# Kernel optimization log

Measured on AMD Instinct MI355X. Metric: run time of the kernel, lower is better.

The kernel has to match this reference:

```python
import jax, jax.numpy as jnp
import numpy as np

NEG_SLOPE = 0.2


def gat_conv(x, src, dst, W, att_src, att_dst, bias, heads, out_dim, concat):
    N = x.shape[0]
    h = (x @ W).reshape(N, heads, out_dim)              # [N,H,F]
    a_src = (h * att_src[None]).sum(-1)                 # [N,H]
    a_dst = (h * att_dst[None]).sum(-1)                 # [N,H]
    e = jax.nn.leaky_relu(a_src[src] + a_dst[dst], NEG_SLOPE)  # [E,H]
    # segment softmax over incoming edges of each dst node
    m = jax.ops.segment_max(e, dst, num_segments=N)     # [N,H]
    p = jnp.exp(e - m[dst])
    s = jax.ops.segment_sum(p, dst, num_segments=N)     # [N,H]
    alpha = p / (s[dst] + 1e-16)                        # [E,H]
    msg = h[src] * alpha[:, :, None]                    # [E,H,F]
    agg = jax.ops.segment_sum(msg, dst, num_segments=N) # [N,H,F]
    if concat:
        out = agg.reshape(N, heads * out_dim)
    else:
        out = agg.mean(axis=1)
    return out + bias


def gat_forward(x, edge_index, W1, att_src1, att_dst1, b1, W2, att_src2, att_dst2, b2):
    N = x.shape[0]
    # add self loops (PyG GATConv default)
    loops = jnp.arange(N, dtype=edge_index.dtype)
    src = jnp.concatenate([edge_index[0], loops])
    dst = jnp.concatenate([edge_index[1], loops])
    h = gat_conv(x, src, dst, W1, att_src1, att_dst1, b1, heads=8, out_dim=8, concat=True)
    h = jax.nn.elu(h)
    # dropout is identity in eval mode
    num_class = W2.shape[1]
    o = gat_conv(h, src, dst, W2, att_src2, att_dst2, b2, heads=1, out_dim=num_class, concat=True)
    return jax.nn.log_softmax(o, axis=-1)


def setup_inputs() -> dict:
    key = jax.random.key(0)
    ks = jax.random.split(key, 8)
    N, E, F_in, C = 100000, 1600000, 128, 40
    H, F_h = 8, 8
    x = jax.random.normal(ks[0], (N, F_in), dtype=jnp.float32)
    edge_index = jax.random.randint(ks[1], (2, E), 0, N, dtype=jnp.int64)
    sc = lambda f: 1.0 / np.sqrt(f)
    W1 = jax.random.normal(ks[2], (F_in, H * F_h), dtype=jnp.float32) * sc(F_in)
    att_src1 = jax.random.normal(ks[3], (H, F_h), dtype=jnp.float32) * sc(F_h)
    att_dst1 = jax.random.normal(ks[4], (H, F_h), dtype=jnp.float32) * sc(F_h)
    b1 = jnp.zeros((H * F_h,), dtype=jnp.float32)
    W2 = jax.random.normal(ks[5], (H * F_h, C), dtype=jnp.float32) * sc(H * F_h)
    att_src2 = jax.random.normal(ks[6], (1, C), dtype=jnp.float32) * sc(C)
    att_dst2 = jax.random.normal(ks[7], (1, C), dtype=jnp.float32) * sc(C)
    b2 = jnp.zeros((C,), dtype=jnp.float32)
    return {"x": x, "edge_index": edge_index, "W1": W1, "att_src1": att_src1,
            "att_dst1": att_dst1, "b1": b1, "W2": W2, "att_src2": att_src2,
            "att_dst2": att_dst2, "b2": b2}


def reference(x, edge_index, W1, att_src1, att_dst1, b1, W2, att_src2, att_dst2, b2):
    return gat_forward(x, edge_index, W1, att_src1, att_dst1, b1, W2, att_src2, att_dst2, b2)
```

## Files before the change

kernel.cpp:

```cpp
#include <hip/hip_runtime.h>
#include <math.h>

#define NEG_SLOPE 0.2f

typedef __attribute__((ext_vector_type(8))) short short8;
typedef __attribute__((ext_vector_type(4))) float f32x4;

__device__ __forceinline__ float leaky(float x) { return x > 0.f ? x : NEG_SLOPE * x; }

__device__ __forceinline__ short f2bf(float f) {
    union { float f; unsigned u; } v; v.f = f;
    unsigned r = v.u + 0x7fffu + ((v.u >> 16) & 1u);
    return (short)(r >> 16);
}
__device__ __forceinline__ float bf2f(unsigned short s) {
    union { unsigned u; float f; } v; v.u = ((unsigned)s) << 16;
    return v.f;
}
__device__ __forceinline__ void unpack2(unsigned v, float& lo, float& hi) {
    union { unsigned u; float f; } a, b;
    a.u = v << 16; b.u = v & 0xffff0000u;
    lo = a.f; hi = b.f;
}

#define GCHUNK 256
#define NB_MAX 1024

__global__ __launch_bounds__(256) void hist_kernel(const int* __restrict__ dst, int E, int nbuck,
                                                   int* __restrict__ histG, int* __restrict__ total) {
    __shared__ int lh[NB_MAX];
    int g = blockIdx.x, t = threadIdx.x;
    for (int i = t; i < nbuck; i += 256) lh[i] = 0;
    __syncthreads();
    int ce = (E + GCHUNK - 1) / GCHUNK;
    int e0 = g * ce, e1 = min(e0 + ce, E);
    for (int e = e0 + t; e < e1; e += 256)
        atomicAdd(&lh[dst[e] >> 7], 1);
    __syncthreads();
    for (int i = t; i < nbuck; i += 256) {
        histG[i * GCHUNK + g] = lh[i];
        if (lh[i]) atomicAdd(&total[i], lh[i]);
    }
}

__global__ __launch_bounds__(1024) void bscan_kernel(const int* __restrict__ total,
                                                     int* __restrict__ bbase, int nbuck) {
    __shared__ int sh[1024];
    int t = threadIdx.x;
    int v = (t < nbuck) ? total[t] : 0;
    sh[t] = v; __syncthreads();
    for (int s = 1; s < 1024; s <<= 1) {
        int add = (t >= s) ? sh[t - s] : 0;
        __syncthreads();
        sh[t] += add;
        __syncthreads();
    }
    if (t < nbuck) bbase[t] = sh[t] - v;
    if (t == nbuck - 1) bbase[nbuck] = sh[t];
}

__global__ __launch_bounds__(256) void bstart_kernel(const int* __restrict__ histG,
                                                     const int* __restrict__ bbase,
                                                     int* __restrict__ startG, int nbuck) {
    __shared__ int sh[256];
    int b = blockIdx.x, t = threadIdx.x;
    int v = histG[b * GCHUNK + t];
    sh[t] = v; __syncthreads();
    for (int s = 1; s < 256; s <<= 1) {
        int add = (t >= s) ? sh[t - s] : 0;
        __syncthreads();
        sh[t] += add;
        __syncthreads();
    }
    startG[b * GCHUNK + t] = bbase[b] + sh[t] - v;
}

__global__ __launch_bounds__(256) void bucket_scatter(const int* __restrict__ src,
                                                      const int* __restrict__ dst, int E, int nbuck,
                                                      const int* __restrict__ startG,
                                                      int* __restrict__ pairbuf) {
    __shared__ int cur[NB_MAX];
    int g = blockIdx.x, t = threadIdx.x;
    for (int i = t; i < nbuck; i += 256) cur[i] = startG[i * GCHUNK + g];
    __syncthreads();
    int ce = (E + GCHUNK - 1) / GCHUNK;
    int e0 = g * ce, e1 = min(e0 + ce, E);
    for (int e = e0 + t; e < e1; e += 256) {
        int d = dst[e], b = d >> 7;
        int pos = atomicAdd(&cur[b], 1);
        pairbuf[pos] = (src[e] << 7) | (d & 127);
    }
}

__global__ __launch_bounds__(256) void bucket_place(const int* __restrict__ pairbuf,
                                                    const int* __restrict__ bbase, int nbuck, int N,
                                                    int* __restrict__ deg, int* __restrict__ off,
                                                    int* __restrict__ csr) {
    __shared__ int stash[4096];
    __shared__ int ldeg[128], lcur[128], sh[128];
    int b = blockIdx.x, t = threadIdx.x;
    int p0 = bbase[b], p1 = bbase[b + 1];
    int cnt = p1 - p0;
    int node0 = b << 7;
    for (int i = t; i < 128; i += 256) ldeg[i] = 0;
    __syncthreads();
    for (int i = t; i < cnt; i += 256) {
        int pr = pairbuf[p0 + i];
        if (i < 4096) stash[i] = pr;
        atomicAdd(&ldeg[pr & 127], 1);
    }
    __syncthreads();
    if (t < 128) sh[t] = ldeg[t];
    __syncthreads();
    for (int s = 1; s < 128; s <<= 1) {
        int add = (t >= s && t < 128) ? sh[t - s] : 0;
        __syncthreads();
        if (t < 128) sh[t] += add;
        __syncthreads();
    }
    if (t < 128) {
        int excl = sh[t] - ldeg[t];
        int n = node0 + t;
        if (n < N) { deg[n] = ldeg[t]; off[n] = p0 + excl; }
        lcur[t] = p0 + excl;
    }
    __syncthreads();
    for (int i = t; i < cnt; i += 256) {
        int pr = (i < 4096) ? stash[i] : pairbuf[p0 + i];
        int pos = atomicAdd(&lcur[pr & 127], 1);
        csr[pos] = ((unsigned)pr) >> 7;
    }
}

__global__ __launch_bounds__(256) void gemm1_mfma(
    const float* __restrict__ x, const float* __restrict__ W1,
    const float* __restrict__ att_src, const float* __restrict__ att_dst,
    unsigned short* __restrict__ h1, float* __restrict__ a_src, float* __restrict__ a_dst, int N)
{
    __shared__ short Bl[16 * 64 * 8];
    __shared__ float Cs[4][32 * 64];
    int tid = threadIdx.x;
    for (int f0 = tid; f0 < 1024; f0 += 256) {
        int lane = f0 & 63, s = (f0 >> 6) & 3, ct = f0 >> 8;
        int kb = s * 32 + ((lane >> 4) << 3);
        int col = ct * 16 + (lane & 15);
        short* dp = &Bl[f0 * 8];
#pragma unroll
        for (int j = 0; j < 8; ++j) dp[j] = f2bf(W1[(kb + j) * 64 + col]);
    }
    __syncthreads();

    int lane = tid & 63, w = tid >> 6;
    int row0 = blockIdx.x * 128 + w * 32;
    int ra = min(row0 + (lane & 15), N - 1);
    int rb = min(row0 + 16 + (lane & 15), N - 1);
    const float* pa = x + (size_t)ra * 128 + ((lane >> 4) << 3);
    const float* pb = x + (size_t)rb * 128 + ((lane >> 4) << 3);

    f32x4 acc[2][4];
#pragma unroll
    for (int i = 0; i < 2; ++i)
#pragma unroll
        for (int j = 0; j < 4; ++j) acc[i][j] = (f32x4){0.f, 0.f, 0.f, 0.f};

#pragma unroll
    for (int s = 0; s < 4; ++s) {
        float4 a0 = *(const float4*)(pa + s * 32);
        float4 a1 = *(const float4*)(pa + s * 32 + 4);
        float4 c0 = *(const float4*)(pb + s * 32);
        float4 c1 = *(const float4*)(pb + s * 32 + 4);
        short8 af, cf;
        af[0] = f2bf(a0.x); af[1] = f2bf(a0.y); af[2] = f2bf(a0.z); af[3] = f2bf(a0.w);
        af[4] = f2bf(a1.x); af[5] = f2bf(a1.y); af[6] = f2bf(a1.z); af[7] = f2bf(a1.w);
        cf[0] = f2bf(c0.x); cf[1] = f2bf(c0.y); cf[2] = f2bf(c0.z); cf[3] = f2bf(c0.w);
        cf[4] = f2bf(c1.x); cf[5] = f2bf(c1.y); cf[6] = f2bf(c1.z); cf[7] = f2bf(c1.w);
#pragma unroll
        for (int ct = 0; ct < 4; ++ct) {
            short8 wf = *(const short8*)&Bl[((ct * 4 + s) * 64 + lane) * 8];
            acc[0][ct] = __builtin_amdgcn_mfma_f32_16x16x32_bf16(af, wf, acc[0][ct], 0, 0, 0);
            acc[1][ct] = __builtin_amdgcn_mfma_f32_16x16x32_bf16(cf, wf, acc[1][ct], 0, 0, 0);
        }
    }

    float* cs = &Cs[w][0];
#pragma unroll
    for (int rt = 0; rt < 2; ++rt)
#pragma unroll
        for (int ct = 0; ct < 4; ++ct)
#pragma unroll
            for (int r = 0; r < 4; ++r) {
                int row = rt * 16 + ((lane >> 4) << 2) + r;
                int col = ct * 16 + (lane & 15);
                cs[row * 64 + col] = acc[rt][ct][r];
            }
    __syncthreads();

    float asv = att_src[lane], adv = att_dst[lane];
    for (int r = 0; r < 32; ++r) {
        int row = row0 + r;
        float v = cs[r * 64 + lane];
        float ts = v * asv, td = v * adv;
        ts += __shfl_xor(ts, 1); ts += __shfl_xor(ts, 2); ts += __shfl_xor(ts, 4);
        td += __shfl_xor(td, 1); td += __shfl_xor(td, 2); td += __shfl_xor(td, 4);
        if (row < N) {
            h1[(size_t)row * 64 + lane] = (unsigned short)f2bf(v);
            if ((lane & 7) == 0) {
                a_src[row * 8 + (lane >> 3)] = ts;
                a_dst[row * 8 + (lane >> 3)] = td;
            }
        }
    }
}

__global__ __launch_bounds__(256) void agg1_kernel(
    const unsigned short* __restrict__ h1, const float* __restrict__ a_src, const float* __restrict__ a_dst,
    const int* __restrict__ off, const int* __restrict__ deg, const int* __restrict__ csr,
    const float* __restrict__ b1, unsigned short* __restrict__ helu, int N)
{
    int tid = threadIdx.x;
    int n = (blockIdx.x * 256 + tid) >> 6;
    int lane = tid & 63;
    if (n >= N) return;
    int o = off[n], d = deg[n];
    int h8 = lane & 7, g = lane >> 3;

    float adst = a_dst[n * 8 + h8];
    float pself = __expf(leaky(a_src[n * 8 + h8] + adst));
    float s = (g == 0) ? pself : 0.f;

    float aself = (g == 0) ? __shfl(pself, h8) : 0.f;
    uint4 dvs = *(const uint4*)(h1 + (size_t)n * 64 + h8 * 8);
    float lo, hi;
    float acc0, acc1, acc2, acc3, acc4, acc5, acc6, acc7;
    unpack2(dvs.x, lo, hi); acc0 = aself * lo; acc1 = aself * hi;
    unpack2(dvs.y, lo, hi); acc2 = aself * lo; acc3 = aself * hi;
    unpack2(dvs.z, lo, hi); acc4 = aself * lo; acc5 = aself * hi;
    unpack2(dvs.w, lo, hi); acc6 = aself * lo; acc7 = aself * hi;

    for (int base = 0; base < d; base += 64) {
        int idx = base + lane;
        int sv = (idx < d) ? csr[o + idx] : 0;
        int lim = min(64, d - base);
        int tmax2 = (((lim + 7) >> 3) + 1) & ~1;
        for (int t = 0; t < tmax2; t += 2) {
            int e0 = t * 8 + g, e1 = e0 + 8;
            int s0 = __shfl(sv, e0), s1 = __shfl(sv, e1);
            float as0 = a_src[s0 * 8 + h8];
            float as1 = a_src[s1 * 8 + h8];
            uint4 d0 = *(const uint4*)(h1 + (size_t)s0 * 64 + h8 * 8);
            uint4 d1 = *(const uint4*)(h1 + (size_t)s1 * 64 + h8 * 8);
            float p0 = (e0 < lim) ? __expf(leaky(as0 + adst)) : 0.f;
            float p1 = (e1 < lim) ? __expf(leaky(as1 + adst)) : 0.f;
            s += p0 + p1;
            unpack2(d0.x, lo, hi); acc0 = fmaf(p0, lo, acc0); acc1 = fmaf(p0, hi, acc1);
            unpack2(d0.y, lo, hi); acc2 = fmaf(p0, lo, acc2); acc3 = fmaf(p0, hi, acc3);
            unpack2(d0.z, lo, hi); acc4 = fmaf(p0, lo, acc4); acc5 = fmaf(p0, hi, acc5);
            unpack2(d0.w, lo, hi); acc6 = fmaf(p0, lo, acc6); acc7 = fmaf(p0, hi, acc7);
            unpack2(d1.x, lo, hi); acc0 = fmaf(p1, lo, acc0); acc1 = fmaf(p1, hi, acc1);
            unpack2(d1.y, lo, hi); acc2 = fmaf(p1, lo, acc2); acc3 = fmaf(p1, hi, acc3);
            unpack2(d1.z, lo, hi); acc4 = fmaf(p1, lo, acc4); acc5 = fmaf(p1, hi, acc5);
            unpack2(d1.w, lo, hi); acc6 = fmaf(p1, lo, acc6); acc7 = fmaf(p1, hi, acc7);
        }
    }
    s += __shfl_xor(s, 8); s += __shfl_xor(s, 16); s += __shfl_xor(s, 32);
    acc0 += __shfl_xor(acc0, 8); acc0 += __shfl_xor(acc0, 16); acc0 += __shfl_xor(acc0, 32);
    acc1 += __shfl_xor(acc1, 8); acc1 += __shfl_xor(acc1, 16); acc1 += __shfl_xor(acc1, 32);
    acc2 += __shfl_xor(acc2, 8); acc2 += __shfl_xor(acc2, 16); acc2 += __shfl_xor(acc2, 32);
    acc3 += __shfl_xor(acc3, 8); acc3 += __shfl_xor(acc3, 16); acc3 += __shfl_xor(acc3, 32);
    acc4 += __shfl_xor(acc4, 8); acc4 += __shfl_xor(acc4, 16); acc4 += __shfl_xor(acc4, 32);
    acc5 += __shfl_xor(acc5, 8); acc5 += __shfl_xor(acc5, 16); acc5 += __shfl_xor(acc5, 32);
    acc6 += __shfl_xor(acc6, 8); acc6 += __shfl_xor(acc6, 16); acc6 += __shfl_xor(acc6, 32);
    acc7 += __shfl_xor(acc7, 8); acc7 += __shfl_xor(acc7, 16); acc7 += __shfl_xor(acc7, 32);

    if (g == 0) {
        float r = 1.f / s;
        float4 bA = *(const float4*)(b1 + h8 * 8);
        float4 bB = *(const float4*)(b1 + h8 * 8 + 4);
        float v0 = acc0 * r + bA.x, v1 = acc1 * r + bA.y;
        float v2 = acc2 * r + bA.z, v3 = acc3 * r + bA.w;
        float v4 = acc4 * r + bB.x, v5 = acc5 * r + bB.y;
        float v6 = acc6 * r + bB.z, v7 = acc7 * r + bB.w;
        v0 = (v0 > 0.f) ? v0 : (__expf(v0) - 1.f);
        v1 = (v1 > 0.f) ? v1 : (__expf(v1) - 1.f);
        v2 = (v2 > 0.f) ? v2 : (__expf(v2) - 1.f);
        v3 = (v3 > 0.f) ? v3 : (__expf(v3) - 1.f);
        v4 = (v4 > 0.f) ? v4 : (__expf(v4) - 1.f);
        v5 = (v5 > 0.f) ? v5 : (__expf(v5) - 1.f);
        v6 = (v6 > 0.f) ? v6 : (__expf(v6) - 1.f);
        v7 = (v7 > 0.f) ? v7 : (__expf(v7) - 1.f);
        uint4 st;
        st.x = ((unsigned)(unsigned short)f2bf(v0)) | (((unsigned)(unsigned short)f2bf(v1)) << 16);
        st.y = ((unsigned)(unsigned short)f2bf(v2)) | (((unsigned)(unsigned short)f2bf(v3)) << 16);
        st.z = ((unsigned)(unsigned short)f2bf(v4)) | (((unsigned)(unsigned short)f2bf(v5)) << 16);
        st.w = ((unsigned)(unsigned short)f2bf(v6)) | (((unsigned)(unsigned short)f2bf(v7)) << 16);
        *(uint4*)(helu + (size_t)n * 64 + h8 * 8) = st;
    }
}

__global__ __launch_bounds__(256) void gemm2_mfma(
    const unsigned short* __restrict__ hin, const float* __restrict__ W2,
    const float* __restrict__ att_src2, const float* __restrict__ att_dst2,
    unsigned short* __restrict__ h2p, float* __restrict__ a_src, float* __restrict__ a_dst, int N)
{
    __shared__ short Bl[6 * 64 * 8];
    __shared__ float Cs[4][32 * 48];
    int tid = threadIdx.x;
    for (int f0 = tid; f0 < 384; f0 += 256) {
        int lane = f0 & 63; int fr = f0 >> 6; int s = fr & 1, ct = fr >> 1;
        int kb = s * 32 + ((lane >> 4) << 3);
        int col = ct * 16 + (lane & 15);
        short* dp = &Bl[f0 * 8];
#pragma unroll
        for (int j = 0; j < 8; ++j) dp[j] = (col < 40) ? f2bf(W2[(kb + j) * 40 + col]) : (short)0;
    }
    __syncthreads();

    int lane = tid & 63, w = tid >> 6;
    int row0 = blockIdx.x * 128 + w * 32;
    int ra = min(row0 + (lane & 15), N - 1);
    int rb = min(row0 + 16 + (lane & 15), N - 1);
    const unsigned short* pa = hin + (size_t)ra * 64 + ((lane >> 4) << 3);
    const unsigned short* pb = hin + (size_t)rb * 64 + ((lane >> 4) << 3);

    f32x4 acc[2][3];
#pragma unroll
    for (int i = 0; i < 2; ++i)
#pragma unroll
        for (int j = 0; j < 3; ++j) acc[i][j] = (f32x4){0.f, 0.f, 0.f, 0.f};

#pragma unroll
    for (int s = 0; s < 2; ++s) {
        short8 af = *(const short8*)(pa + s * 32);
        short8 cf = *(const short8*)(pb + s * 32);
#pragma unroll
        for (int ct = 0; ct < 3; ++ct) {
            short8 wf = *(const short8*)&Bl[((ct * 2 + s) * 64 + lane) * 8];
            acc[0][ct] = __builtin_amdgcn_mfma_f32_16x16x32_bf16(af, wf, acc[0][ct], 0, 0, 0);
            acc[1][ct] = __builtin_amdgcn_mfma_f32_16x16x32_bf16(cf, wf, acc[1][ct], 0, 0, 0);
        }
    }

    float* cs = &Cs[w][0];
#pragma unroll
    for (int rt = 0; rt < 2; ++rt)
#pragma unroll
        for (int ct = 0; ct < 3; ++ct)
#pragma unroll
            for (int r = 0; r < 4; ++r) {
                int row = rt * 16 + ((lane >> 4) << 2) + r;
                int col = ct * 16 + (lane & 15);
                cs[row * 48 + col] = acc[rt][ct][r];
            }
    __syncthreads();

    float asv = (lane < 40) ? att_src2[lane] : 0.f;
    float adv = (lane < 40) ? att_dst2[lane] : 0.f;
    for (int r = 0; r < 32; ++r) {
        int row = row0 + r;
        float v = (lane < 48) ? cs[r * 48 + lane] : 0.f;
        float ts = (lane < 40) ? v * asv : 0.f;
        float td = (lane < 40) ? v * adv : 0.f;
        for (int st = 1; st < 64; st <<= 1) { ts += __shfl_xor(ts, st); td += __shfl_xor(td, st); }
        if (row < N) {
            h2p[(size_t)row * 64 + lane] = (unsigned short)f2bf(v);
            if (lane == 0) { a_src[row] = ts; a_dst[row] = td; }
        }
    }
}

__global__ __launch_bounds__(256) void agg2_kernel(
    const unsigned short* __restrict__ h2p, const float* __restrict__ a_src, const float* __restrict__ a_dst,
    const int* __restrict__ off, const int* __restrict__ deg, const int* __restrict__ csr,
    const float* __restrict__ b2, float* __restrict__ out, int N)
{
    int tid = threadIdx.x;
    int n = (blockIdx.x * 256 + tid) >> 6;
    int lane = tid & 63;
    if (n >= N) return;
    int o = off[n], d = deg[n];
    int h8 = lane & 7, g = lane >> 3;

    float adst = a_dst[n];
    float pself = __expf(leaky(a_src[n] + adst));
    float sp = (g == 0) ? pself : 0.f;

    float aself = (g == 0) ? pself : 0.f;
    uint4 dvs = *(const uint4*)(h2p + (size_t)n * 64 + h8 * 8);
    float lo, hi;
    float acc0, acc1, acc2, acc3, acc4, acc5, acc6, acc7;
    unpack2(dvs.x, lo, hi); acc0 = aself * lo; acc1 = aself * hi;
    unpack2(dvs.y, lo, hi); acc2 = aself * lo; acc3 = aself * hi;
    unpack2(dvs.z, lo, hi); acc4 = aself * lo; acc5 = aself * hi;
    unpack2(dvs.w, lo, hi); acc6 = aself * lo; acc7 = aself * hi;

    for (int base = 0; base < d; base += 64) {
        int idx = base + lane;
        int sv = (idx < d) ? csr[o + idx] : 0;
        int lim = min(64, d - base);
        int tmax2 = (((lim + 7) >> 3) + 1) & ~1;
        for (int t = 0; t < tmax2; t += 2) {
            int e0 = t * 8 + g, e1 = e0 + 8;
            int s0 = __shfl(sv, e0), s1 = __shfl(sv, e1);
            float as0 = a_src[s0];
            float as1 = a_src[s1];
            uint4 d0 = *(const uint4*)(h2p + (size_t)s0 * 64 + h8 * 8);
            uint4 d1 = *(const uint4*)(h2p + (size_t)s1 * 64 + h8 * 8);
            float p0 = (e0 < lim) ? __expf(leaky(as0 + adst)) : 0.f;
            float p1 = (e1 < lim) ? __expf(leaky(as1 + adst)) : 0.f;
            sp += p0 + p1;
            unpack2(d0.x, lo, hi); acc0 = fmaf(p0, lo, acc0); acc1 = fmaf(p0, hi, acc1);
            unpack2(d0.y, lo, hi); acc2 = fmaf(p0, lo, acc2); acc3 = fmaf(p0, hi, acc3);
            unpack2(d0.z, lo, hi); acc4 = fmaf(p0, lo, acc4); acc5 = fmaf(p0, hi, acc5);
            unpack2(d0.w, lo, hi); acc6 = fmaf(p0, lo, acc6); acc7 = fmaf(p0, hi, acc7);
            unpack2(d1.x, lo, hi); acc0 = fmaf(p1, lo, acc0); acc1 = fmaf(p1, hi, acc1);
            unpack2(d1.y, lo, hi); acc2 = fmaf(p1, lo, acc2); acc3 = fmaf(p1, hi, acc3);
            unpack2(d1.z, lo, hi); acc4 = fmaf(p1, lo, acc4); acc5 = fmaf(p1, hi, acc5);
            unpack2(d1.w, lo, hi); acc6 = fmaf(p1, lo, acc6); acc7 = fmaf(p1, hi, acc7);
        }
    }
    sp += __shfl_xor(sp, 8); sp += __shfl_xor(sp, 16); sp += __shfl_xor(sp, 32);
    acc0 += __shfl_xor(acc0, 8); acc0 += __shfl_xor(acc0, 16); acc0 += __shfl_xor(acc0, 32);
    acc1 += __shfl_xor(acc1, 8); acc1 += __shfl_xor(acc1, 16); acc1 += __shfl_xor(acc1, 32);
    acc2 += __shfl_xor(acc2, 8); acc2 += __shfl_xor(acc2, 16); acc2 += __shfl_xor(acc2, 32);
    acc3 += __shfl_xor(acc3, 8); acc3 += __shfl_xor(acc3, 16); acc3 += __shfl_xor(acc3, 32);
    acc4 += __shfl_xor(acc4, 8); acc4 += __shfl_xor(acc4, 16); acc4 += __shfl_xor(acc4, 32);
    acc5 += __shfl_xor(acc5, 8); acc5 += __shfl_xor(acc5, 16); acc5 += __shfl_xor(acc5, 32);
    acc6 += __shfl_xor(acc6, 8); acc6 += __shfl_xor(acc6, 16); acc6 += __shfl_xor(acc6, 32);
    acc7 += __shfl_xor(acc7, 8); acc7 += __shfl_xor(acc7, 16); acc7 += __shfl_xor(acc7, 32);

    if (g == 0) {
        float r = 1.f / sp;
        float v0 = -INFINITY, v1 = -INFINITY, v2 = -INFINITY, v3 = -INFINITY;
        float v4 = -INFINITY, v5 = -INFINITY, v6 = -INFINITY, v7 = -INFINITY;
        if (h8 < 5) {
            float4 bA = *(const float4*)(b2 + h8 * 8);
            float4 bB = *(const float4*)(b2 + h8 * 8 + 4);
            v0 = acc0 * r + bA.x; v1 = acc1 * r + bA.y;
            v2 = acc2 * r + bA.z; v3 = acc3 * r + bA.w;
            v4 = acc4 * r + bB.x; v5 = acc5 * r + bB.y;
            v6 = acc6 * r + bB.z; v7 = acc7 * r + bB.w;
        }
        float mx = fmaxf(fmaxf(fmaxf(v0, v1), fmaxf(v2, v3)), fmaxf(fmaxf(v4, v5), fmaxf(v6, v7)));
        mx = fmaxf(mx, __shfl_xor(mx, 1));
        mx = fmaxf(mx, __shfl_xor(mx, 2));
        mx = fmaxf(mx, __shfl_xor(mx, 4));
        float se = 0.f;
        if (h8 < 5)
            se = __expf(v0 - mx) + __expf(v1 - mx) + __expf(v2 - mx) + __expf(v3 - mx)
               + __expf(v4 - mx) + __expf(v5 - mx) + __expf(v6 - mx) + __expf(v7 - mx);
        se += __shfl_xor(se, 1); se += __shfl_xor(se, 2); se += __shfl_xor(se, 4);
        if (h8 < 5) {
            float ls = mx + logf(se);
            float* op = out + (size_t)n * 40 + h8 * 8;
            *(float4*)op = make_float4(v0 - ls, v1 - ls, v2 - ls, v3 - ls);
            *(float4*)(op + 4) = make_float4(v4 - ls, v5 - ls, v6 - ls, v7 - ls);
        }
    }
}

extern "C" void kernel_launch(void* const* d_in, const int* in_sizes, int n_in,
                              void* d_out, int out_size, void* d_ws, size_t ws_size,
                              hipStream_t stream) {
    const float* x        = (const float*)d_in[0];
    const int*   ei       = (const int*)d_in[1];
    const float* W1       = (const float*)d_in[2];
    const float* att_src1 = (const float*)d_in[3];
    const float* att_dst1 = (const float*)d_in[4];
    const float* b1       = (const float*)d_in[5];
    const float* W2       = (const float*)d_in[6];
    const float* att_src2 = (const float*)d_in[7];
    const float* att_dst2 = (const float*)d_in[8];
    const float* b2       = (const float*)d_in[9];
    float* out = (float*)d_out;

    int N = in_sizes[0] / 128;
    int E = in_sizes[1] / 2;
    const int* src = ei;
    const int* dst = ei + E;
    int nbuck = (N + 127) >> 7;

    char* w = (char*)d_ws;
    auto alloc = [&](size_t bytes) { void* p = (void*)w; w += (bytes + 255) & ~(size_t)255; return p; };
    unsigned short* h1   = (unsigned short*)alloc((size_t)N * 64 * 2);
    unsigned short* helu = (unsigned short*)alloc((size_t)N * 64 * 2);
    float* as1  = (float*)alloc((size_t)N * 8 * 4);
    float* ad1  = (float*)alloc((size_t)N * 8 * 4);
    int*   degv = (int*)alloc((size_t)N * 4);
    int*   offv = (int*)alloc((size_t)(N + 1) * 4);
    int*   csr  = (int*)alloc((size_t)E * 4);
    int*   histG  = (int*)alloc((size_t)nbuck * GCHUNK * 4);
    int*   startG = (int*)alloc((size_t)nbuck * GCHUNK * 4);
    int*   total  = (int*)alloc((size_t)nbuck * 4);
    int*   bbase  = (int*)alloc((size_t)(nbuck + 1) * 4);
    int*   pairbuf = (int*)alloc((size_t)E * 4);
    unsigned short* h2p = h1;
    float* as2 = as1;
    float* ad2 = ad1;

    hipMemsetAsync(total, 0, (size_t)nbuck * 4, stream);
    hist_kernel<<<GCHUNK, 256, 0, stream>>>(dst, E, nbuck, histG, total);
    bscan_kernel<<<1, 1024, 0, stream>>>(total, bbase, nbuck);
    bstart_kernel<<<nbuck, 256, 0, stream>>>(histG, bbase, startG, nbuck);
    bucket_scatter<<<GCHUNK, 256, 0, stream>>>(src, dst, E, nbuck, startG, pairbuf);
    bucket_place<<<nbuck, 256, 0, stream>>>(pairbuf, bbase, nbuck, N, degv, offv, csr);

    int gb = (N + 127) / 128;
    gemm1_mfma<<<gb, 256, 0, stream>>>(x, W1, att_src1, att_dst1, h1, as1, ad1, N);
    agg1_kernel<<<(N + 3) / 4, 256, 0, stream>>>(h1, as1, ad1, offv, degv, csr, b1, helu, N);
    gemm2_mfma<<<gb, 256, 0, stream>>>(helu, W2, att_src2, att_dst2, h2p, as2, ad2, N);
    agg2_kernel<<<(N + 3) / 4, 256, 0, stream>>>(h2p, as2, ad2, offv, degv, csr, b2, out, N);
}
```

Measured before the change: 327.5 us.

## Map one graph node per half-wavefront in both aggregation kernels

Both aggregation kernels now give each destination node 32 lanes instead of a full 64-lane wavefront. There are 4 edge groups of 8 head or feature lanes, and the grid launches half as many blocks. With about 16 incoming edges per node, the old mapping left many lanes idle and spent a third butterfly-reduction stage. Packing two nodes per wavefront should raise lane utilization and cut shuffle work. The cost is a longer serial edge loop per group, plus an odd-step tail and a conditional self-loop load.

```diff
diff --git a/kernel.cpp b/kernel.cpp
--- a/kernel.cpp
+++ b/kernel.cpp
@@ -218,33 +218,38 @@
     const float* __restrict__ b1, unsigned short* __restrict__ helu, int N)
 {
     int tid = threadIdx.x;
-    int n = (blockIdx.x * 256 + tid) >> 6;
+    int n = (blockIdx.x * 256 + tid) >> 5;
     int lane = tid & 63;
+    int l32 = lane & 31;
+    int hb = lane & 32;
     if (n >= N) return;
     int o = off[n], d = deg[n];
-    int h8 = lane & 7, g = lane >> 3;
+    int h8 = l32 & 7, g = l32 >> 3;
 
     float adst = a_dst[n * 8 + h8];
     float pself = __expf(leaky(a_src[n * 8 + h8] + adst));
     float s = (g == 0) ? pself : 0.f;
 
-    float aself = (g == 0) ? __shfl(pself, h8) : 0.f;
-    uint4 dvs = *(const uint4*)(h1 + (size_t)n * 64 + h8 * 8);
     float lo, hi;
-    float acc0, acc1, acc2, acc3, acc4, acc5, acc6, acc7;
-    unpack2(dvs.x, lo, hi); acc0 = aself * lo; acc1 = aself * hi;
-    unpack2(dvs.y, lo, hi); acc2 = aself * lo; acc3 = aself * hi;
-    unpack2(dvs.z, lo, hi); acc4 = aself * lo; acc5 = aself * hi;
-    unpack2(dvs.w, lo, hi); acc6 = aself * lo; acc7 = aself * hi;
-
-    for (int base = 0; base < d; base += 64) {
-        int idx = base + lane;
+    float acc0 = 0.f, acc1 = 0.f, acc2 = 0.f, acc3 = 0.f;
+    float acc4 = 0.f, acc5 = 0.f, acc6 = 0.f, acc7 = 0.f;
+    if (g == 0) {
+        uint4 dvs = *(const uint4*)(h1 + (size_t)n * 64 + h8 * 8);
+        unpack2(dvs.x, lo, hi); acc0 = pself * lo; acc1 = pself * hi;
+        unpack2(dvs.y, lo, hi); acc2 = pself * lo; acc3 = pself * hi;
+        unpack2(dvs.z, lo, hi); acc4 = pself * lo; acc5 = pself * hi;
+        unpack2(dvs.w, lo, hi); acc6 = pself * lo; acc7 = pself * hi;
+    }
+
+    for (int base = 0; base < d; base += 32) {
+        int idx = base + l32;
         int sv = (idx < d) ? csr[o + idx] : 0;
-        int lim = min(64, d - base);
-        int tmax2 = (((lim + 7) >> 3) + 1) & ~1;
-        for (int t = 0; t < tmax2; t += 2) {
-            int e0 = t * 8 + g, e1 = e0 + 8;
-            int s0 = __shfl(sv, e0), s1 = __shfl(sv, e1);
+        int lim = min(32, d - base);
+        int tm = (lim + 3) >> 2;
+        int t = 0;
+        for (; t + 1 < tm; t += 2) {
+            int e0 = t * 4 + g, e1 = e0 + 4;
+            int s0 = __shfl(sv, hb | e0), s1 = __shfl(sv, hb | e1);
             float as0 = a_src[s0 * 8 + h8];
             float as1 = a_src[s1 * 8 + h8];
             uint4 d0 = *(const uint4*)(h1 + (size_t)s0 * 64 + h8 * 8);
@@ -261,16 +266,28 @@
             unpack2(d1.z, lo, hi); acc4 = fmaf(p1, lo, acc4); acc5 = fmaf(p1, hi, acc5);
             unpack2(d1.w, lo, hi); acc6 = fmaf(p1, lo, acc6); acc7 = fmaf(p1, hi, acc7);
         }
-    }
-    s += __shfl_xor(s, 8); s += __shfl_xor(s, 16); s += __shfl_xor(s, 32);
-    acc0 += __shfl_xor(acc0, 8); acc0 += __shfl_xor(acc0, 16); acc0 += __shfl_xor(acc0, 32);
-    acc1 += __shfl_xor(acc1, 8); acc1 += __shfl_xor(acc1, 16); acc1 += __shfl_xor(acc1, 32);
-    acc2 += __shfl_xor(acc2, 8); acc2 += __shfl_xor(acc2, 16); acc2 += __shfl_xor(acc2, 32);
-    acc3 += __shfl_xor(acc3, 8); acc3 += __shfl_xor(acc3, 16); acc3 += __shfl_xor(acc3, 32);
-    acc4 += __shfl_xor(acc4, 8); acc4 += __shfl_xor(acc4, 16); acc4 += __shfl_xor(acc4, 32);
-    acc5 += __shfl_xor(acc5, 8); acc5 += __shfl_xor(acc5, 16); acc5 += __shfl_xor(acc5, 32);
-    acc6 += __shfl_xor(acc6, 8); acc6 += __shfl_xor(acc6, 16); acc6 += __shfl_xor(acc6, 32);
-    acc7 += __shfl_xor(acc7, 8); acc7 += __shfl_xor(acc7, 16); acc7 += __shfl_xor(acc7, 32);
+        if (t < tm) {
+            int e0 = t * 4 + g;
+            int s0 = __shfl(sv, hb | e0);
+            float as0 = a_src[s0 * 8 + h8];
+            uint4 d0 = *(const uint4*)(h1 + (size_t)s0 * 64 + h8 * 8);
+            float p0 = (e0 < lim) ? __expf(leaky(as0 + adst)) : 0.f;
+            s += p0;
+            unpack2(d0.x, lo, hi); acc0 = fmaf(p0, lo, acc0); acc1 = fmaf(p0, hi, acc1);
+            unpack2(d0.y, lo, hi); acc2 = fmaf(p0, lo, acc2); acc3 = fmaf(p0, hi, acc3);
+            unpack2(d0.z, lo, hi); acc4 = fmaf(p0, lo, acc4); acc5 = fmaf(p0, hi, acc5);
+            unpack2(d0.w, lo, hi); acc6 = fmaf(p0, lo, acc6); acc7 = fmaf(p0, hi, acc7);
+        }
+    }
+    s += __shfl_xor(s, 8); s += __shfl_xor(s, 16);
+    acc0 += __shfl_xor(acc0, 8); acc0 += __shfl_xor(acc0, 16);
+    acc1 += __shfl_xor(acc1, 8); acc1 += __shfl_xor(acc1, 16);
+    acc2 += __shfl_xor(acc2, 8); acc2 += __shfl_xor(acc2, 16);
+    acc3 += __shfl_xor(acc3, 8); acc3 += __shfl_xor(acc3, 16);
+    acc4 += __shfl_xor(acc4, 8); acc4 += __shfl_xor(acc4, 16);
+    acc5 += __shfl_xor(acc5, 8); acc5 += __shfl_xor(acc5, 16);
+    acc6 += __shfl_xor(acc6, 8); acc6 += __shfl_xor(acc6, 16);
+    acc7 += __shfl_xor(acc7, 8); acc7 += __shfl_xor(acc7, 16);
 
     if (g == 0) {
         float r = 1.f / s;
@@ -374,33 +391,38 @@
     const float* __restrict__ b2, float* __restrict__ out, int N)
 {
     int tid = threadIdx.x;
-    int n = (blockIdx.x * 256 + tid) >> 6;
+    int n = (blockIdx.x * 256 + tid) >> 5;
     int lane = tid & 63;
+    int l32 = lane & 31;
+    int hb = lane & 32;
     if (n >= N) return;
     int o = off[n], d = deg[n];
-    int h8 = lane & 7, g = lane >> 3;
+    int h8 = l32 & 7, g = l32 >> 3;
 
     float adst = a_dst[n];
     float pself = __expf(leaky(a_src[n] + adst));
     float sp = (g == 0) ? pself : 0.f;
 
-    float aself = (g == 0) ? pself : 0.f;
-    uint4 dvs = *(const uint4*)(h2p + (size_t)n * 64 + h8 * 8);
     float lo, hi;
-    float acc0, acc1, acc2, acc3, acc4, acc5, acc6, acc7;
-    unpack2(dvs.x, lo, hi); acc0 = aself * lo; acc1 = aself * hi;
-    unpack2(dvs.y, lo, hi); acc2 = aself * lo; acc3 = aself * hi;
-    unpack2(dvs.z, lo, hi); acc4 = aself * lo; acc5 = aself * hi;
-    unpack2(dvs.w, lo, hi); acc6 = aself * lo; acc7 = aself * hi;
-
-    for (int base = 0; base < d; base += 64) {
-        int idx = base + lane;
+    float acc0 = 0.f, acc1 = 0.f, acc2 = 0.f, acc3 = 0.f;
+    float acc4 = 0.f, acc5 = 0.f, acc6 = 0.f, acc7 = 0.f;
+    if (g == 0) {
+        uint4 dvs = *(const uint4*)(h2p + (size_t)n * 64 + h8 * 8);
+        unpack2(dvs.x, lo, hi); acc0 = pself * lo; acc1 = pself * hi;
+        unpack2(dvs.y, lo, hi); acc2 = pself * lo; acc3 = pself * hi;
+        unpack2(dvs.z, lo, hi); acc4 = pself * lo; acc5 = pself * hi;
+        unpack2(dvs.w, lo, hi); acc6 = pself * lo; acc7 = pself * hi;
+    }
+
+    for (int base = 0; base < d; base += 32) {
+        int idx = base + l32;
         int sv = (idx < d) ? csr[o + idx] : 0;
-        int lim = min(64, d - base);
-        int tmax2 = (((lim + 7) >> 3) + 1) & ~1;
-        for (int t = 0; t < tmax2; t += 2) {
-            int e0 = t * 8 + g, e1 = e0 + 8;
-            int s0 = __shfl(sv, e0), s1 = __shfl(sv, e1);
+        int lim = min(32, d - base);
+        int tm = (lim + 3) >> 2;
+        int t = 0;
+        for (; t + 1 < tm; t += 2) {
+            int e0 = t * 4 + g, e1 = e0 + 4;
+            int s0 = __shfl(sv, hb | e0), s1 = __shfl(sv, hb | e1);
             float as0 = a_src[s0];
             float as1 = a_src[s1];
             uint4 d0 = *(const uint4*)(h2p + (size_t)s0 * 64 + h8 * 8);
@@ -417,16 +439,28 @@
             unpack2(d1.z, lo, hi); acc4 = fmaf(p1, lo, acc4); acc5 = fmaf(p1, hi, acc5);
             unpack2(d1.w, lo, hi); acc6 = fmaf(p1, lo, acc6); acc7 = fmaf(p1, hi, acc7);
         }
-    }
-    sp += __shfl_xor(sp, 8); sp += __shfl_xor(sp, 16); sp += __shfl_xor(sp, 32);
-    acc0 += __shfl_xor(acc0, 8); acc0 += __shfl_xor(acc0, 16); acc0 += __shfl_xor(acc0, 32);
-    acc1 += __shfl_xor(acc1, 8); acc1 += __shfl_xor(acc1, 16); acc1 += __shfl_xor(acc1, 32);
-    acc2 += __shfl_xor(acc2, 8); acc2 += __shfl_xor(acc2, 16); acc2 += __shfl_xor(acc2, 32);
-    acc3 += __shfl_xor(acc3, 8); acc3 += __shfl_xor(acc3, 16); acc3 += __shfl_xor(acc3, 32);
-    acc4 += __shfl_xor(acc4, 8); acc4 += __shfl_xor(acc4, 16); acc4 += __shfl_xor(acc4, 32);
-    acc5 += __shfl_xor(acc5, 8); acc5 += __shfl_xor(acc5, 16); acc5 += __shfl_xor(acc5, 32);
-    acc6 += __shfl_xor(acc6, 8); acc6 += __shfl_xor(acc6, 16); acc6 += __shfl_xor(acc6, 32);
-    acc7 += __shfl_xor(acc7, 8); acc7 += __shfl_xor(acc7, 16); acc7 += __shfl_xor(acc7, 32);
+        if (t < tm) {
+            int e0 = t * 4 + g;
+            int s0 = __shfl(sv, hb | e0);
+            float as0 = a_src[s0];
+            uint4 d0 = *(const uint4*)(h2p + (size_t)s0 * 64 + h8 * 8);
+            float p0 = (e0 < lim) ? __expf(leaky(as0 + adst)) : 0.f;
+            sp += p0;
+            unpack2(d0.x, lo, hi); acc0 = fmaf(p0, lo, acc0); acc1 = fmaf(p0, hi, acc1);
+            unpack2(d0.y, lo, hi); acc2 = fmaf(p0, lo, acc2); acc3 = fmaf(p0, hi, acc3);
+            unpack2(d0.z, lo, hi); acc4 = fmaf(p0, lo, acc4); acc5 = fmaf(p0, hi, acc5);
+            unpack2(d0.w, lo, hi); acc6 = fmaf(p0, lo, acc6); acc7 = fmaf(p0, hi, acc7);
+        }
+    }
+    sp += __shfl_xor(sp, 8); sp += __shfl_xor(sp, 16);
+    acc0 += __shfl_xor(acc0, 8); acc0 += __shfl_xor(acc0, 16);
+    acc1 += __shfl_xor(acc1, 8); acc1 += __shfl_xor(acc1, 16);
+    acc2 += __shfl_xor(acc2, 8); acc2 += __shfl_xor(acc2, 16);
+    acc3 += __shfl_xor(acc3, 8); acc3 += __shfl_xor(acc3, 16);
+    acc4 += __shfl_xor(acc4, 8); acc4 += __shfl_xor(acc4, 16);
+    acc5 += __shfl_xor(acc5, 8); acc5 += __shfl_xor(acc5, 16);
+    acc6 += __shfl_xor(acc6, 8); acc6 += __shfl_xor(acc6, 16);
+    acc7 += __shfl_xor(acc7, 8); acc7 += __shfl_xor(acc7, 16);
 
     if (g == 0) {
         float r = 1.f / sp;
@@ -506,7 +540,7 @@
 
     int gb = (N + 127) / 128;
     gemm1_mfma<<<gb, 256, 0, stream>>>(x, W1, att_src1, att_dst1, h1, as1, ad1, N);
-    agg1_kernel<<<(N + 3) / 4, 256, 0, stream>>>(h1, as1, ad1, offv, degv, csr, b1, helu, N);
+    agg1_kernel<<<(N + 7) / 8, 256, 0, stream>>>(h1, as1, ad1, offv, degv, csr, b1, helu, N);
     gemm2_mfma<<<gb, 256, 0, stream>>>(helu, W2, att_src2, att_dst2, h2p, as2, ad2, N);
-    agg2_kernel<<<(N + 3) / 4, 256, 0, stream>>>(h2p, as2, ad2, offv, degv, csr, b2, out, N);
-}
+    agg2_kernel<<<(N + 7) / 8, 256, 0, stream>>>(h2p, as2, ad2, offv, degv, csr, b2, out, N);
+}
```

Measured after the change: 291.9 us. -10.9%, faster.
